# Kernel tuning notes

Hardware: AMD Instinct MI355X
Metric: run time of the kernel (lower is better)

The kernel has to match this reference:

```python
import jax, jax.numpy as jnp
import numpy as np

B, N, C = 16, 2048, 512
NUM_HEADS = 8
D = C // NUM_HEADS  # 64


def setup_inputs() -> dict:
    key = jax.random.key(0)
    ks = jax.random.split(key, 8)
    s = 0.02
    return {
        "x": jax.random.normal(ks[0], (B, N, C), dtype=jnp.float32),
        "Wq": jax.random.normal(ks[1], (D, C), dtype=jnp.float32) * s,
        "bq": jax.random.normal(ks[2], (D,), dtype=jnp.float32) * s,
        "Wk": jax.random.normal(ks[3], (D, C), dtype=jnp.float32) * s,
        "bk": jax.random.normal(ks[4], (D,), dtype=jnp.float32) * s,
        "Wv": jax.random.normal(ks[5], (C, C), dtype=jnp.float32) * s,
        "bv": jax.random.normal(ks[6], (C,), dtype=jnp.float32) * s,
        "gamma": jax.random.normal(ks[7], (1,), dtype=jnp.float32) * 0.1,
    }


def reference(x, Wq, bq, Wk, bk, Wv, bv, gamma):
    # x: [B, N, C]; torch code permutes to [B, C, N] (channels for Conv1d)
    xt = jnp.transpose(x, (0, 2, 1))                      # [B, C, N]
    # 1x1 Conv1d == pointwise linear over channel dim
    q = jnp.einsum('dc,bcn->bdn', Wq, xt) + bq[None, :, None]   # [B, D, N]
    k = jnp.einsum('dc,bcn->bdn', Wk, xt) + bk[None, :, None]   # [B, D, N]
    v = jnp.einsum('oc,bcn->bon', Wv, xt) + bv[None, :, None]   # [B, C, N]
    # energy[b, n, m] = <q[:, n], k[:, m]>
    energy = jnp.einsum('bdn,bdm->bnm', q, k)             # [B, N, N]
    attention = jax.nn.softmax(energy, axis=-1)           # [B, N, N]
    # out = bmm(v, attention^T): out[b, c, n] = sum_m v[b, c, m] * attn[b, n, m]
    out = jnp.einsum('bcm,bnm->bcn', v, attention)        # [B, C, N]
    out = gamma[0] * out + xt
    return jnp.transpose(out, (0, 2, 1))                  # [B, N, C]
```

## Files before the change

kernel.cpp:

```cpp
#include <hip/hip_runtime.h>
#include <hip/hip_bf16.h>

typedef __bf16 bf16x8 __attribute__((ext_vector_type(8)));
typedef float f32x4 __attribute__((ext_vector_type(4)));

#define B_ 16
#define N_ 2048
#define C_ 512
#define D_ 64

__device__ __forceinline__ float bf2f(ushort u) {
    union { uint i; float f; } w; w.i = ((uint)u) << 16; return w.f;
}
__device__ __forceinline__ ushort f2bf(float f) {
    union { float f; uint i; } w; w.f = f;
    uint u = w.i;
    u = (u + 0x7fffu + ((u >> 16) & 1u)) >> 16;
    return (ushort)u;
}
__device__ __forceinline__ __bf16 u2b(ushort u) {
    union { ushort s; __bf16 b; } w; w.s = u; return w.b;
}
__device__ __forceinline__ bf16x8 ld8u(const ushort* p) { return *(const bf16x8*)p; }
__device__ __forceinline__ bf16x8 ld8f(const float* p) {
    f32x4 a = *(const f32x4*)p;
    f32x4 b = *(const f32x4*)(p + 4);
    bf16x8 r;
    r[0] = u2b(f2bf(a[0])); r[1] = u2b(f2bf(a[1]));
    r[2] = u2b(f2bf(a[2])); r[3] = u2b(f2bf(a[3]));
    r[4] = u2b(f2bf(b[0])); r[5] = u2b(f2bf(b[1]));
    r[6] = u2b(f2bf(b[2])); r[7] = u2b(f2bf(b[3]));
    return r;
}

__device__ __forceinline__ void gload16(const ushort* g, ushort* l) {
    __builtin_amdgcn_global_load_lds(
        (const __attribute__((address_space(1))) void*)g,
        (__attribute__((address_space(3))) void*)l, 16, 0, 0);
}

__global__ void probe_kernel(const void* x, int* flag) {
    int lane = threadIdx.x & 63;
    ushort u = ((const ushort*)x)[lane * 2];
    float v = fabsf(bf2f(u));
    bool sane = (v > 9.3e-10f) && (v < 1.1e9f) && (v == v);
    unsigned long long m = __ballot(sane);
    if (threadIdx.x == 0) *flag = (__popcll(m) >= 48) ? 0 : 1;
}

__launch_bounds__(256, 2)
__global__ void proj_qk_kernel(const void* __restrict__ X,
                               const void* __restrict__ Wq_,
                               const void* __restrict__ bq_,
                               const void* __restrict__ Wk_,
                               const void* __restrict__ bk_,
                               ushort* __restrict__ outq,
                               ushort* __restrict__ outk,
                               const int* __restrict__ flag) {
    const int isf32 = *flag;
    const ushort* Xu  = (const ushort*)X;
    const float*  Xf  = (const float*)X;
    const ushort* Wqu = (const ushort*)Wq_;
    const float*  Wqf = (const float*)Wq_;
    const ushort* Wku = (const ushort*)Wk_;
    const float*  Wkf = (const float*)Wk_;
    const ushort* Bqu = (const ushort*)bq_;
    const float*  Bqf = (const float*)bq_;
    const ushort* Bku = (const ushort*)bk_;
    const float*  Bkf = (const float*)bk_;

    __shared__ ushort lA[64][72];
    __shared__ ushort lBq[64][72];
    __shared__ ushort lBk[64][72];
    const int tid  = threadIdx.x;
    const int wave = tid >> 6, lane = tid & 63;
    const int quad = lane >> 4, li = lane & 15;
    const int m0 = blockIdx.x * 64;

    f32x4 accq[4], acck[4];
    #pragma unroll
    for (int t = 0; t < 4; ++t) {
        accq[t] = (f32x4){0.f, 0.f, 0.f, 0.f};
        acck[t] = (f32x4){0.f, 0.f, 0.f, 0.f};
    }

    for (int k0 = 0; k0 < C_; k0 += 64) {
        __syncthreads();
        #pragma unroll
        for (int it = 0; it < 2; ++it) {
            int idx = tid + it * 256;
            int row = idx >> 3, seg = idx & 7;
            size_t ea = (size_t)(m0 + row) * C_ + k0 + seg * 8;
            size_t eb = (size_t)row * C_ + k0 + seg * 8;
            if (!isf32) {
                *(bf16x8*)&lA[row][seg * 8]  = ld8u(Xu + ea);
                *(bf16x8*)&lBq[row][seg * 8] = ld8u(Wqu + eb);
                *(bf16x8*)&lBk[row][seg * 8] = ld8u(Wku + eb);
            } else {
                *(bf16x8*)&lA[row][seg * 8]  = ld8f(Xf + ea);
                *(bf16x8*)&lBq[row][seg * 8] = ld8f(Wqf + eb);
                *(bf16x8*)&lBk[row][seg * 8] = ld8f(Wkf + eb);
            }
        }
        __syncthreads();
        #pragma unroll
        for (int ks = 0; ks < 2; ++ks) {
            bf16x8 a = *(const bf16x8*)&lA[wave * 16 + li][ks * 32 + quad * 8];
            #pragma unroll
            for (int t = 0; t < 4; ++t) {
                bf16x8 bq8 = *(const bf16x8*)&lBq[t * 16 + li][ks * 32 + quad * 8];
                bf16x8 bk8 = *(const bf16x8*)&lBk[t * 16 + li][ks * 32 + quad * 8];
                accq[t] = __builtin_amdgcn_mfma_f32_16x16x32_bf16(a, bq8, accq[t], 0, 0, 0);
                acck[t] = __builtin_amdgcn_mfma_f32_16x16x32_bf16(a, bk8, acck[t], 0, 0, 0);
            }
        }
    }

    #pragma unroll
    for (int t = 0; t < 4; ++t) {
        int c = t * 16 + li;
        float bvq = isf32 ? Bqf[c] : bf2f(Bqu[c]);
        float bvk = isf32 ? Bkf[c] : bf2f(Bku[c]);
        #pragma unroll
        for (int j = 0; j < 4; ++j) {
            int m = m0 + wave * 16 + quad * 4 + j;
            outq[(size_t)m * D_ + c] = f2bf(accq[t][j] + bvq);
            outk[(size_t)m * D_ + c] = f2bf(acck[t][j] + bvk);
        }
    }
}

template<int NCOLS, int MODE>
__launch_bounds__(256, 2)
__global__ void proj_kernel(const void* __restrict__ X,
                            const void* __restrict__ W,
                            const void* __restrict__ bias,
                            ushort* __restrict__ out,
                            const int* __restrict__ flag,
                            size_t xoff) {
    const int isf32 = *flag;
    const ushort* Xu = (const ushort*)X + xoff;
    const float*  Xf = (const float*)X + xoff;
    const ushort* Wu = (const ushort*)W;
    const float*  Wf = (const float*)W;
    const ushort* Bu = (const ushort*)bias;
    const float*  Bf = (const float*)bias;

    __shared__ ushort lA[64][72];
    __shared__ ushort lB[64][72];
    const int tid  = threadIdx.x;
    const int wave = tid >> 6, lane = tid & 63;
    const int quad = lane >> 4, li = lane & 15;
    const int m0 = blockIdx.x * 64;
    const int n0 = blockIdx.y * 64;

    f32x4 acc[4];
    #pragma unroll
    for (int t = 0; t < 4; ++t) acc[t] = (f32x4){0.f, 0.f, 0.f, 0.f};

    for (int k0 = 0; k0 < C_; k0 += 64) {
        __syncthreads();
        #pragma unroll
        for (int it = 0; it < 2; ++it) {
            int idx = tid + it * 256;
            int row = idx >> 3, seg = idx & 7;
            size_t ea = (size_t)(m0 + row) * C_ + k0 + seg * 8;
            size_t eb = (size_t)(n0 + row) * C_ + k0 + seg * 8;
            if (!isf32) {
                *(bf16x8*)&lA[row][seg * 8] = ld8u(Xu + ea);
                *(bf16x8*)&lB[row][seg * 8] = ld8u(Wu + eb);
            } else {
                *(bf16x8*)&lA[row][seg * 8] = ld8f(Xf + ea);
                *(bf16x8*)&lB[row][seg * 8] = ld8f(Wf + eb);
            }
        }
        __syncthreads();
        #pragma unroll
        for (int ks = 0; ks < 2; ++ks) {
            bf16x8 a = *(const bf16x8*)&lA[wave * 16 + li][ks * 32 + quad * 8];
            #pragma unroll
            for (int t = 0; t < 4; ++t) {
                bf16x8 b = *(const bf16x8*)&lB[t * 16 + li][ks * 32 + quad * 8];
                acc[t] = __builtin_amdgcn_mfma_f32_16x16x32_bf16(a, b, acc[t], 0, 0, 0);
            }
        }
    }

    #pragma unroll
    for (int t = 0; t < 4; ++t) {
        int c = n0 + t * 16 + li;
        float bv = isf32 ? Bf[c] : bf2f(Bu[c]);
        if (MODE == 0) {
            #pragma unroll
            for (int j = 0; j < 4; ++j) {
                int m = m0 + wave * 16 + quad * 4 + j;
                out[(size_t)m * NCOLS + c] = f2bf(acc[t][j] + bv);
            }
        } else {
            int m = m0 + wave * 16 + quad * 4;
            int b = m >> 11, ml = m & (N_ - 1);
            ushort4 pk;
            pk.x = f2bf(acc[t][0] + bv);
            pk.y = f2bf(acc[t][1] + bv);
            pk.z = f2bf(acc[t][2] + bv);
            pk.w = f2bf(acc[t][3] + bv);
            *(ushort4*)(out + ((size_t)(b * C_ + c)) * N_ + ml) = pk;
        }
    }
}

__launch_bounds__(512, 4)
__global__ void attn_fused(const ushort* __restrict__ q,
                           const ushort* __restrict__ kk,
                           const ushort* __restrict__ vt,
                           const void* __restrict__ x,
                           const void* __restrict__ gptr,
                           void* __restrict__ out,
                           const int* __restrict__ flag) {
    __shared__ ushort Pl[64 * 64];
    __shared__ ushort Vl[256 * 64];
    __shared__ ushort Kl[64 * 64];
    __shared__ float  ll[64];

    const int tid  = threadIdx.x;
    const int wave = tid >> 6, lane = tid & 63;
    const int quad = lane >> 4, li = lane & 15;
    const int wq = wave & 1;
    const int wm = wave >> 1;
    const int b  = blockIdx.z;
    const int q0 = blockIdx.x * 64;
    const int c0 = blockIdx.y * 256;

    const ushort* kb = kk + (size_t)b * N_ * D_;
    const ushort* vb = vt + ((size_t)b * C_ + c0) * N_;

    const int lrow8 = lane >> 3;
    const int lseg  = (lane & 7) ^ lrow8;

    bf16x8 qf[2][2];
    #pragma unroll
    for (int i = 0; i < 2; ++i)
        #pragma unroll
        for (int ks = 0; ks < 2; ++ks)
            qf[i][ks] = ld8u(q + ((size_t)(b * N_ + q0 + wq * 32 + i * 16 + li)) * D_
                               + ks * 32 + quad * 8);

    f32x4 acc[2][4];
    #pragma unroll
    for (int i = 0; i < 2; ++i)
        #pragma unroll
        for (int j = 0; j < 4; ++j) acc[i][j] = (f32x4){0.f, 0.f, 0.f, 0.f};

    f32x4 accp[2];
    float s4[2][4];
    #pragma unroll
    for (int i = 0; i < 2; ++i) {
        accp[i] = (f32x4){0.f, 0.f, 0.f, 0.f};
        #pragma unroll
        for (int j = 0; j < 4; ++j) s4[i][j] = 0.f;
    }

    #pragma unroll
    for (int ks = 0; ks < 2; ++ks) {
        bf16x8 kf = ld8u(kb + ((size_t)(wm * 16 + li)) * D_ + ks * 32 + quad * 8);
        #pragma unroll
        for (int i = 0; i < 2; ++i)
            accp[i] = __builtin_amdgcn_mfma_f32_16x16x32_bf16(qf[i][ks], kf, accp[i], 0, 0, 0);
    }

    for (int t = 0; t < 32; ++t) {
        __syncthreads();
        #pragma unroll
        for (int it = 0; it < 4; ++it) {
            int rbase = wave * 32 + it * 8;
            gload16(vb + (size_t)(rbase + lrow8) * N_ + t * 64 + lseg * 8,
                    &Vl[rbase * 64]);
        }
        if (t < 31) {
            int rbase = wave * 8;
            gload16(kb + (size_t)((t + 1) * 64 + rbase + lrow8) * D_ + lseg * 8,
                    &Kl[rbase * 64]);
        }
        #pragma unroll
        for (int i = 0; i < 2; ++i)
            #pragma unroll
            for (int j = 0; j < 4; ++j) {
                int r = wq * 32 + i * 16 + quad * 4 + j;
                int m = wm * 16 + li;
                float e = __expf(fminf(accp[i][j], 60.f));
                s4[i][j] += e;
                Pl[r * 64 + (((m >> 3) ^ (r & 7)) * 8) + (m & 7)] = f2bf(e);
            }
        __syncthreads();

        if (t < 31) {
            #pragma unroll
            for (int i = 0; i < 2; ++i) accp[i] = (f32x4){0.f, 0.f, 0.f, 0.f};
            #pragma unroll
            for (int ks = 0; ks < 2; ++ks) {
                bf16x8 kf = *(const bf16x8*)&Kl[(wm * 16 + li) * 64
                                                + (((ks * 4 + quad) ^ (li & 7)) * 8)];
                #pragma unroll
                for (int i = 0; i < 2; ++i)
                    accp[i] = __builtin_amdgcn_mfma_f32_16x16x32_bf16(
                        qf[i][ks], kf, accp[i], 0, 0, 0);
            }
        }

        #pragma unroll
        for (int ks = 0; ks < 2; ++ks) {
            bf16x8 af[2];
            #pragma unroll
            for (int i = 0; i < 2; ++i)
                af[i] = *(const bf16x8*)&Pl[(wq * 32 + i * 16 + li) * 64
                                            + (((ks * 4 + quad) ^ (li & 7)) * 8)];
            #pragma unroll
            for (int j = 0; j < 4; ++j) {
                bf16x8 vf = *(const bf16x8*)&Vl[(wm * 64 + j * 16 + li) * 64
                                                + (((ks * 4 + quad) ^ (li & 7)) * 8)];
                #pragma unroll
                for (int i = 0; i < 2; ++i)
                    acc[i][j] = __builtin_amdgcn_mfma_f32_16x16x32_bf16(
                        af[i], vf, acc[i][j], 0, 0, 0);
            }
        }
    }

    __syncthreads();
    if (tid < 64) ll[tid] = 0.f;
    __syncthreads();
    #pragma unroll
    for (int i = 0; i < 2; ++i)
        #pragma unroll
        for (int j = 0; j < 4; ++j) {
            float s = s4[i][j];
            s += __shfl_xor(s, 1, 64);
            s += __shfl_xor(s, 2, 64);
            s += __shfl_xor(s, 4, 64);
            s += __shfl_xor(s, 8, 64);
            if (li == 0) atomicAdd(&ll[wq * 32 + i * 16 + quad * 4 + j], s);
        }
    __syncthreads();

    const int isf32 = *flag;
    const float g = isf32 ? ((const float*)gptr)[0] : bf2f(((const ushort*)gptr)[0]);
    const ushort* xu = (const ushort*)x;
    const float*  xf = (const float*)x;
    ushort* ou = (ushort*)out;
    float*  of = (float*)out;
    #pragma unroll
    for (int i = 0; i < 2; ++i)
        #pragma unroll
        for (int jj = 0; jj < 4; ++jj) {
            int nl = wq * 32 + i * 16 + quad * 4 + jj;
            float inv = 1.f / ll[nl];
            size_t rowb = ((size_t)(b * N_ + q0 + nl)) * C_;
            #pragma unroll
            for (int j = 0; j < 4; ++j) {
                int cg = c0 + wm * 64 + j * 16 + li;
                size_t idx = rowb + cg;
                float xv  = isf32 ? xf[idx] : bf2f(xu[idx]);
                float val = g * (acc[i][j][jj] * inv) + xv;
                if (isf32) of[idx] = val; else ou[idx] = f2bf(val);
            }
        }
}

extern "C" void kernel_launch(void* const* d_in, const int* in_sizes, int n_in,
                              void* d_out, int out_size, void* d_ws, size_t ws_size,
                              hipStream_t stream) {
    (void)in_sizes; (void)n_in; (void)out_size; (void)ws_size;
    const void* x     = d_in[0];
    const void* Wq    = d_in[1];
    const void* bq    = d_in[2];
    const void* Wk    = d_in[3];
    const void* bk    = d_in[4];
    const void* Wv    = d_in[5];
    const void* bv    = d_in[6];
    const void* gamma = d_in[7];

    int*    flag = (int*)d_ws;
    ushort* q    = (ushort*)((char*)d_ws + 256);
    ushort* kk   = q  + (size_t)B_ * N_ * D_;
    ushort* vt   = kk + (size_t)B_ * N_ * D_;

    probe_kernel<<<1, 64, 0, stream>>>(x, flag);

    const int M = B_ * N_;
    proj_qk_kernel<<<dim3(M / 64), 256, 0, stream>>>(x, Wq, bq, Wk, bk, q, kk, flag);
    proj_kernel<C_, 1><<<dim3(M / 64, C_ / 64), 256, 0, stream>>>(
        x, Wv, bv, vt, flag, 0);
    attn_fused<<<dim3(N_ / 64, 2, B_), 512, 0, stream>>>(
        q, kk, vt, x, gamma, d_out, flag);
}
```

Measured before the change: 333.4 us.

## Double-buffer V tiles in LDS and prefetch K into registers

The attention loop now double-buffers the V tile in shared memory, issuing the async load for tile t+1 while tile t is consumed. K fragments move from an LDS staging buffer to registers loaded two steps ahead. Barriers become explicit s_waitcnt/s_barrier pairs with sched_barrier fences and raised priority around the PV MFMAs. This is meant to hide global load latency behind compute. In exchange, LDS use rises to about 74 KB, which may cut occupancy below the launch_bounds target, and the hand-counted vmcnt values must match the number of outstanding loads exactly.

```diff
diff --git a/kernel.cpp b/kernel.cpp
--- a/kernel.cpp
+++ b/kernel.cpp
@@ -217,9 +217,8 @@
                            const void* __restrict__ gptr,
                            void* __restrict__ out,
                            const int* __restrict__ flag) {
+    __shared__ ushort Vl[2][256 * 64];
     __shared__ ushort Pl[64 * 64];
-    __shared__ ushort Vl[256 * 64];
-    __shared__ ushort Kl[64 * 64];
     __shared__ float  ll[64];
 
     const int tid  = threadIdx.x;
@@ -261,25 +260,30 @@
     }
 
     #pragma unroll
-    for (int ks = 0; ks < 2; ++ks) {
-        bf16x8 kf = ld8u(kb + ((size_t)(wm * 16 + li)) * D_ + ks * 32 + quad * 8);
-        #pragma unroll
-        for (int i = 0; i < 2; ++i)
-            accp[i] = __builtin_amdgcn_mfma_f32_16x16x32_bf16(qf[i][ks], kf, accp[i], 0, 0, 0);
-    }
+    for (int it = 0; it < 4; ++it) {
+        int rbase = wave * 32 + it * 8;
+        gload16(vb + (size_t)(rbase + lrow8) * N_ + lseg * 8, &Vl[0][rbase * 64]);
+    }
+    {
+        bf16x8 k0 = ld8u(kb + (size_t)(wm * 16 + li) * D_ + quad * 8);
+        bf16x8 k1 = ld8u(kb + (size_t)(wm * 16 + li) * D_ + 32 + quad * 8);
+        accp[0] = __builtin_amdgcn_mfma_f32_16x16x32_bf16(qf[0][0], k0, accp[0], 0, 0, 0);
+        accp[1] = __builtin_amdgcn_mfma_f32_16x16x32_bf16(qf[1][0], k0, accp[1], 0, 0, 0);
+        accp[0] = __builtin_amdgcn_mfma_f32_16x16x32_bf16(qf[0][1], k1, accp[0], 0, 0, 0);
+        accp[1] = __builtin_amdgcn_mfma_f32_16x16x32_bf16(qf[1][1], k1, accp[1], 0, 0, 0);
+    }
+    bf16x8 kreg0 = ld8u(kb + (size_t)(64 + wm * 16 + li) * D_ + quad * 8);
+    bf16x8 kreg1 = ld8u(kb + (size_t)(64 + wm * 16 + li) * D_ + 32 + quad * 8);
 
     for (int t = 0; t < 32; ++t) {
-        __syncthreads();
-        #pragma unroll
-        for (int it = 0; it < 4; ++it) {
-            int rbase = wave * 32 + it * 8;
-            gload16(vb + (size_t)(rbase + lrow8) * N_ + t * 64 + lseg * 8,
-                    &Vl[rbase * 64]);
-        }
+        const int cur = t & 1;
         if (t < 31) {
-            int rbase = wave * 8;
-            gload16(kb + (size_t)((t + 1) * 64 + rbase + lrow8) * D_ + lseg * 8,
-                    &Kl[rbase * 64]);
+            #pragma unroll
+            for (int it = 0; it < 4; ++it) {
+                int rbase = wave * 32 + it * 8;
+                gload16(vb + (size_t)(rbase + lrow8) * N_ + (t + 1) * 64 + lseg * 8,
+                        &Vl[cur ^ 1][rbase * 64]);
+            }
         }
         #pragma unroll
         for (int i = 0; i < 2; ++i)
@@ -289,24 +293,30 @@
                 int m = wm * 16 + li;
                 float e = __expf(fminf(accp[i][j], 60.f));
                 s4[i][j] += e;
-                Pl[r * 64 + (((m >> 3) ^ (r & 7)) * 8) + (m & 7)] = f2bf(e);
-            }
-        __syncthreads();
-
+                *(__bf16*)&Pl[r * 64 + (((m >> 3) ^ (r & 7)) * 8) + (m & 7)] = (__bf16)e;
+            }
         if (t < 31) {
-            #pragma unroll
-            for (int i = 0; i < 2; ++i) accp[i] = (f32x4){0.f, 0.f, 0.f, 0.f};
-            #pragma unroll
-            for (int ks = 0; ks < 2; ++ks) {
-                bf16x8 kf = *(const bf16x8*)&Kl[(wm * 16 + li) * 64
-                                                + (((ks * 4 + quad) ^ (li & 7)) * 8)];
-                #pragma unroll
-                for (int i = 0; i < 2; ++i)
-                    accp[i] = __builtin_amdgcn_mfma_f32_16x16x32_bf16(
-                        qf[i][ks], kf, accp[i], 0, 0, 0);
-            }
-        }
-
+            f32x4 np0 = (f32x4){0.f, 0.f, 0.f, 0.f};
+            f32x4 np1 = (f32x4){0.f, 0.f, 0.f, 0.f};
+            np0 = __builtin_amdgcn_mfma_f32_16x16x32_bf16(qf[0][0], kreg0, np0, 0, 0, 0);
+            np1 = __builtin_amdgcn_mfma_f32_16x16x32_bf16(qf[1][0], kreg0, np1, 0, 0, 0);
+            np0 = __builtin_amdgcn_mfma_f32_16x16x32_bf16(qf[0][1], kreg1, np0, 0, 0, 0);
+            np1 = __builtin_amdgcn_mfma_f32_16x16x32_bf16(qf[1][1], kreg1, np1, 0, 0, 0);
+            if (t < 30) {
+                kreg0 = ld8u(kb + (size_t)((t + 2) * 64 + wm * 16 + li) * D_ + quad * 8);
+                kreg1 = ld8u(kb + (size_t)((t + 2) * 64 + wm * 16 + li) * D_ + 32 + quad * 8);
+            }
+            accp[0] = np0;
+            accp[1] = np1;
+        }
+        if (t < 30)       asm volatile("s_waitcnt vmcnt(6) lgkmcnt(0)" ::: "memory");
+        else if (t == 30) asm volatile("s_waitcnt vmcnt(4) lgkmcnt(0)" ::: "memory");
+        else              asm volatile("s_waitcnt vmcnt(0) lgkmcnt(0)" ::: "memory");
+        __builtin_amdgcn_sched_barrier(0);
+        __builtin_amdgcn_s_barrier();
+        __builtin_amdgcn_sched_barrier(0);
+
+        __builtin_amdgcn_s_setprio(1);
         #pragma unroll
         for (int ks = 0; ks < 2; ++ks) {
             bf16x8 af[2];
@@ -316,14 +326,19 @@
                                             + (((ks * 4 + quad) ^ (li & 7)) * 8)];
             #pragma unroll
             for (int j = 0; j < 4; ++j) {
-                bf16x8 vf = *(const bf16x8*)&Vl[(wm * 64 + j * 16 + li) * 64
-                                                + (((ks * 4 + quad) ^ (li & 7)) * 8)];
+                bf16x8 vf = *(const bf16x8*)&Vl[cur][(wm * 64 + j * 16 + li) * 64
+                                                    + (((ks * 4 + quad) ^ (li & 7)) * 8)];
                 #pragma unroll
                 for (int i = 0; i < 2; ++i)
                     acc[i][j] = __builtin_amdgcn_mfma_f32_16x16x32_bf16(
                         af[i], vf, acc[i][j], 0, 0, 0);
             }
         }
+        __builtin_amdgcn_s_setprio(0);
+
+        __builtin_amdgcn_sched_barrier(0);
+        __builtin_amdgcn_s_barrier();
+        __builtin_amdgcn_sched_barrier(0);
     }
 
     __syncthreads();
```

Result: no change. 330.1 us (-1.0%).
